# Performance work log

Measured on AMD Instinct MI355X. Metric: run time of the kernel, lower is better.

Reference implementation:

```python
import jax, jax.numpy as jnp
import numpy as np

T_VALUES = [0.015, 0.06, 0.25, 1.0]
EPS = 1e-05
SR_OVER_HOP = 44100.0 / 512.0  # frames per second


def _s_values():
    t = np.asarray(T_VALUES, dtype=np.float32) * SR_OVER_HOP
    s = (np.sqrt(1.0 + 4.0 * t ** 2) - 1.0) / (2.0 * t ** 2)
    return jnp.asarray(s, dtype=jnp.float32)  # (n_s,)


def setup_inputs() -> dict:
    key = jax.random.key(0)
    k1, = jax.random.split(key, 1)
    B, F, T = 16, 128, 4096
    # non-negative energies (spectrogram magnitudes)
    x = jax.random.uniform(k1, (B, F, T), dtype=jnp.float32) * 10.0
    alpha_log = jnp.full((F,), float(np.log(0.8)), dtype=jnp.float32)
    delta_log = jnp.full((F,), float(np.log(10.0)), dtype=jnp.float32)
    r_log = jnp.full((F,), float(np.log(0.25)), dtype=jnp.float32)
    return {"x": x, "alpha_log": alpha_log, "delta_log": delta_log, "r_log": r_log}


def reference(x, alpha_log, delta_log, r_log):
    # x: (B, F, T)
    s = _s_values()                      # (n_s,)
    s_b = s[:, None, None]               # (n_s, 1, 1)
    B, F, T = x.shape
    n_s = s.shape[0]

    # Multi-rate EMA over time (first-order IIR), init with first frame.
    xs = jnp.moveaxis(x, -1, 0)          # (T, B, F)
    m0 = jnp.broadcast_to(xs[0][None], (n_s, B, F))

    def step(m, xt):
        m = (1.0 - s_b) * m + s_b * xt[None]  # (n_s, B, F)
        return m, m

    _, m_rest = jax.lax.scan(step, m0, xs[1:])          # (T-1, n_s, B, F)
    m_seq = jnp.concatenate([m0[None], m_rest], axis=0)  # (T, n_s, B, F)
    smoother = jnp.moveaxis(m_seq, 0, -1)                # (n_s, B, F, T)

    alpha = jnp.exp(alpha_log)[None, None, :, None]      # per band
    delta = jnp.exp(delta_log)[None, None, :, None]
    r = jnp.exp(r_log)[None, None, :, None]

    log_eps = jnp.log(jnp.asarray(EPS, dtype=x.dtype))
    smooth = jnp.exp(-alpha * (log_eps + jnp.log1p(smoother / EPS)))
    pcen = (x[None] * smooth + delta) ** r - delta ** r   # (n_s, B, F, T)
    return jnp.transpose(pcen, (1, 0, 2, 3))              # (B, n_s, F, T)
```

## Files before the change

kernel.cpp:

```cpp
#include <hip/hip_runtime.h>


#define EPS_C 1e-5f

__device__ __forceinline__ float fexp2(float v) { return __builtin_amdgcn_exp2f(v); }
__device__ __forceinline__ float flog2(float v) { return __builtin_amdgcn_logf(v); }
__device__ __forceinline__ float fpow(float a, float b) { return fexp2(b * flog2(a)); }
__device__ __forceinline__ float fexp(float v) { return fexp2(v * 1.44269504f); }

__global__ __launch_bounds__(256, 6)
void pcen_kernel(const float* __restrict__ x,
                 const float* __restrict__ alpha_log,
                 const float* __restrict__ delta_log,
                 const float* __restrict__ r_log,
                 float* __restrict__ out)
{
    const int row  = blockIdx.x;
    const int f    = row & 127;
    const int b    = row >> 7;
    const int tid  = threadIdx.x;
    const int lane = tid & 63;
    const int w    = tid >> 6;

    __shared__ float wq[4][4];
    __shared__ float sh_x0;

    const float4* __restrict__ xrow4 = (const float4*)(x + (size_t)row * 4096);
    float xs[16];
#pragma unroll
    for (int k = 0; k < 4; ++k) {
        float4 v = xrow4[4 * tid + k];
        xs[4*k+0] = v.x; xs[4*k+1] = v.y; xs[4*k+2] = v.z; xs[4*k+3] = v.w;
    }
    if (tid == 0) sh_x0 = xs[0];

    const float Tv[4] = {0.015f, 0.06f, 0.25f, 1.0f};
    float s_arr[4], omn_arr[4];
#pragma unroll
    for (int i = 0; i < 4; ++i) {
        float t  = Tv[i] * 86.1328125f;
        float t2 = t * t;
        float s  = (__builtin_sqrtf(1.0f + 4.0f * t2) - 1.0f) / (2.0f * t2);
        s_arr[i]   = s;
        omn_arr[i] = 1.0f - s;
    }

    float qxv[4];
#pragma unroll
    for (int i = 0; i < 4; ++i) {
        const float s = s_arr[i], omn = omn_arr[i];
        float p = 0.0f;
#pragma unroll
        for (int j = 0; j < 16; ++j) p = fmaf(omn, p, s * xs[j]);
        float c = omn * omn;
        c = c * c; c = c * c; c = c * c;
        float q = p;
#pragma unroll
        for (int k = 0; k < 6; ++k) {
            int d = 1 << k;
            float tsh = __shfl_up(q, d);
            if (lane >= d) q = fmaf(c, tsh, q);
            c = c * c;
        }
        float qx = __shfl_up(q, 1);
        if (lane == 0) qx = 0.0f;
        qxv[i] = qx;
        if (lane == 63) wq[i][w] = q;
    }

    const float al = alpha_log[f], dlg = delta_log[f], rl = r_log[f];
    const float nalpha  = -fexp(al);
    const float delta   =  fexp(dlg);
    const float r       =  fexp(rl);
    const float delta_r =  fexp(r * dlg);

    __syncthreads();
    const float x0 = sh_x0;

    float4* __restrict__ out4 = (float4*)out;

#pragma unroll
    for (int i = 0; i < 4; ++i) {
        const float s = s_arr[i], omn = omn_arr[i];
        const float l2omn = flog2(omn);
        const float Dw = fexp2(1024.0f * l2omn);
        float Q = x0;
        for (int v = 0; v < w; ++v) Q = fmaf(Dw, Q, wq[i][v]);
        const float dlane = fexp2((float)(16 * lane) * l2omn);
        float m = fmaf(dlane, Q, qxv[i]);
        const size_t obase4 = ((size_t)((b * 4 + i) * 128 + f)) * 1024 + 4 * tid;
#pragma unroll
        for (int k = 0; k < 4; ++k) {
            float4 o;
            m = fmaf(omn, m, s * xs[4*k+0]);
            o.x = fpow(fmaf(xs[4*k+0], fpow(EPS_C + m, nalpha), delta), r) - delta_r;
            m = fmaf(omn, m, s * xs[4*k+1]);
            o.y = fpow(fmaf(xs[4*k+1], fpow(EPS_C + m, nalpha), delta), r) - delta_r;
            m = fmaf(omn, m, s * xs[4*k+2]);
            o.z = fpow(fmaf(xs[4*k+2], fpow(EPS_C + m, nalpha), delta), r) - delta_r;
            m = fmaf(omn, m, s * xs[4*k+3]);
            o.w = fpow(fmaf(xs[4*k+3], fpow(EPS_C + m, nalpha), delta), r) - delta_r;
            out4[obase4 + k] = o;
        }
    }
}

extern "C" void kernel_launch(void* const* d_in, const int* in_sizes, int n_in,
                              void* d_out, int out_size, void* d_ws, size_t ws_size,
                              hipStream_t stream) {
    const float* x  = (const float*)d_in[0];
    const float* al = (const float*)d_in[1];
    const float* dl = (const float*)d_in[2];
    const float* rl = (const float*)d_in[3];
    float* out = (float*)d_out;
    const int rows = in_sizes[0] / 4096;
    pcen_kernel<<<rows, 256, 0, stream>>>(x, al, dl, rl, out);
}
```

Baseline: 177.9 us.

## Assign one smoothing rate per wave and drop cross-wave LDS scan

Restructures the kernel so each of the four waves handles one EMA rate over the full 4096-sample row, with each lane scanning 64 contiguous samples. The per-wave LDS combine and block barrier go away, and x is reloaded from global memory in the output pass instead of being kept in registers. The occupancy hint is raised to 8. The cost is strided per-lane memory access and repeated reads of the input row.

```diff
diff --git a/kernel.cpp b/kernel.cpp
--- a/kernel.cpp
+++ b/kernel.cpp
@@ -8,7 +8,7 @@
 __device__ __forceinline__ float fpow(float a, float b) { return fexp2(b * flog2(a)); }
 __device__ __forceinline__ float fexp(float v) { return fexp2(v * 1.44269504f); }
 
-__global__ __launch_bounds__(256, 6)
+__global__ __launch_bounds__(256, 8)
 void pcen_kernel(const float* __restrict__ x,
                  const float* __restrict__ alpha_log,
                  const float* __restrict__ delta_log,
@@ -22,51 +22,43 @@
     const int lane = tid & 63;
     const int w    = tid >> 6;
 
-    __shared__ float wq[4][4];
-    __shared__ float sh_x0;
+    const float Tv = (w == 0) ? 0.015f : (w == 1) ? 0.06f : (w == 2) ? 0.25f : 1.0f;
+    const float t   = Tv * 86.1328125f;
+    const float t2  = t * t;
+    const float s   = (__builtin_sqrtf(1.0f + 4.0f * t2) - 1.0f) / (2.0f * t2);
+    const float omn = 1.0f - s;
 
     const float4* __restrict__ xrow4 = (const float4*)(x + (size_t)row * 4096);
-    float xs[16];
+
+    float p = 0.0f;
+    float xfirst = 0.0f;
 #pragma unroll
-    for (int k = 0; k < 4; ++k) {
-        float4 v = xrow4[4 * tid + k];
-        xs[4*k+0] = v.x; xs[4*k+1] = v.y; xs[4*k+2] = v.z; xs[4*k+3] = v.w;
+    for (int k = 0; k < 16; ++k) {
+        float4 v = xrow4[lane * 16 + k];
+        if (k == 0) xfirst = v.x;
+        p = fmaf(omn, p, s * v.x);
+        p = fmaf(omn, p, s * v.y);
+        p = fmaf(omn, p, s * v.z);
+        p = fmaf(omn, p, s * v.w);
     }
-    if (tid == 0) sh_x0 = xs[0];
+    const float x0 = __shfl(xfirst, 0);
 
-    const float Tv[4] = {0.015f, 0.06f, 0.25f, 1.0f};
-    float s_arr[4], omn_arr[4];
+    float c = omn * omn;
+    c = c * c; c = c * c; c = c * c; c = c * c; c = c * c;
+    float q = p;
 #pragma unroll
-    for (int i = 0; i < 4; ++i) {
-        float t  = Tv[i] * 86.1328125f;
-        float t2 = t * t;
-        float s  = (__builtin_sqrtf(1.0f + 4.0f * t2) - 1.0f) / (2.0f * t2);
-        s_arr[i]   = s;
-        omn_arr[i] = 1.0f - s;
+    for (int k = 0; k < 6; ++k) {
+        int d = 1 << k;
+        float tsh = __shfl_up(q, d);
+        if (lane >= d) q = fmaf(c, tsh, q);
+        c = c * c;
     }
+    float qx = __shfl_up(q, 1);
+    if (lane == 0) qx = 0.0f;
 
-    float qxv[4];
-#pragma unroll
-    for (int i = 0; i < 4; ++i) {
-        const float s = s_arr[i], omn = omn_arr[i];
-        float p = 0.0f;
-#pragma unroll
-        for (int j = 0; j < 16; ++j) p = fmaf(omn, p, s * xs[j]);
-        float c = omn * omn;
-        c = c * c; c = c * c; c = c * c;
-        float q = p;
-#pragma unroll
-        for (int k = 0; k < 6; ++k) {
-            int d = 1 << k;
-            float tsh = __shfl_up(q, d);
-            if (lane >= d) q = fmaf(c, tsh, q);
-            c = c * c;
-        }
-        float qx = __shfl_up(q, 1);
-        if (lane == 0) qx = 0.0f;
-        qxv[i] = qx;
-        if (lane == 63) wq[i][w] = q;
-    }
+    const float l2omn = flog2(omn);
+    const float dlane = fexp2((float)(64 * lane) * l2omn);
+    float m = fmaf(dlane, x0, qx);
 
     const float al = alpha_log[f], dlg = delta_log[f], rl = r_log[f];
     const float nalpha  = -fexp(al);
@@ -74,34 +66,22 @@
     const float r       =  fexp(rl);
     const float delta_r =  fexp(r * dlg);
 
-    __syncthreads();
-    const float x0 = sh_x0;
-
-    float4* __restrict__ out4 = (float4*)out;
+    float4* __restrict__ out4 =
+        (float4*)(out + (((size_t)(b * 4 + w)) * 128 + f) * 4096);
 
 #pragma unroll
-    for (int i = 0; i < 4; ++i) {
-        const float s = s_arr[i], omn = omn_arr[i];
-        const float l2omn = flog2(omn);
-        const float Dw = fexp2(1024.0f * l2omn);
-        float Q = x0;
-        for (int v = 0; v < w; ++v) Q = fmaf(Dw, Q, wq[i][v]);
-        const float dlane = fexp2((float)(16 * lane) * l2omn);
-        float m = fmaf(dlane, Q, qxv[i]);
-        const size_t obase4 = ((size_t)((b * 4 + i) * 128 + f)) * 1024 + 4 * tid;
-#pragma unroll
-        for (int k = 0; k < 4; ++k) {
-            float4 o;
-            m = fmaf(omn, m, s * xs[4*k+0]);
-            o.x = fpow(fmaf(xs[4*k+0], fpow(EPS_C + m, nalpha), delta), r) - delta_r;
-            m = fmaf(omn, m, s * xs[4*k+1]);
-            o.y = fpow(fmaf(xs[4*k+1], fpow(EPS_C + m, nalpha), delta), r) - delta_r;
-            m = fmaf(omn, m, s * xs[4*k+2]);
-            o.z = fpow(fmaf(xs[4*k+2], fpow(EPS_C + m, nalpha), delta), r) - delta_r;
-            m = fmaf(omn, m, s * xs[4*k+3]);
-            o.w = fpow(fmaf(xs[4*k+3], fpow(EPS_C + m, nalpha), delta), r) - delta_r;
-            out4[obase4 + k] = o;
-        }
+    for (int k = 0; k < 16; ++k) {
+        float4 v = xrow4[lane * 16 + k];
+        float4 o;
+        m = fmaf(omn, m, s * v.x);
+        o.x = fpow(fmaf(v.x, fpow(EPS_C + m, nalpha), delta), r) - delta_r;
+        m = fmaf(omn, m, s * v.y);
+        o.y = fpow(fmaf(v.y, fpow(EPS_C + m, nalpha), delta), r) - delta_r;
+        m = fmaf(omn, m, s * v.z);
+        o.z = fpow(fmaf(v.z, fpow(EPS_C + m, nalpha), delta), r) - delta_r;
+        m = fmaf(omn, m, s * v.w);
+        o.w = fpow(fmaf(v.w, fpow(EPS_C + m, nalpha), delta), r) - delta_r;
+        out4[lane * 16 + k] = o;
     }
 }
 
```

After: 340.8 us. 1.92x slower.
